# Kernel optimization log

Hardware: AMD Instinct MI355X
Metric: run time of the kernel (lower is better)

## Reference

```python
import jax, jax.numpy as jnp
import numpy as np

STRIDE = 1  # conv stride from __init__


def setup_inputs() -> dict:
    key = jax.random.key(0)
    k1, k2, k3 = jax.random.split(key, 3)
    prot1 = jax.random.normal(k1, (4, 1024, 8, 64), dtype=jnp.float32)
    prot2 = jax.random.normal(k2, (4, 1024, 8, 64), dtype=jnp.float32)
    # W: (no_filters, no_channels, no_dims, window_size)
    W = jax.random.normal(k3, (32, 8, 64, 7), dtype=jnp.float32)
    return {"prot1": prot1, "prot2": prot2, "W": W}


def _project(x, W, stride):
    """Fused equivalent of unfold + broadcast-mul + sum over (C, window).

    x: (N, H, C, D), W: (F, C, D, w) -> (N, F, H', D) with H' = (H - w)//stride + 1.
    This is a grouped 1D conv: D groups, each mixing C input channels into F outputs.
    """
    N, H, C, D = x.shape
    Fn, _, _, w = W.shape
    xg = jnp.transpose(x, (0, 3, 2, 1)).reshape(N, D * C, H)        # (N, D*C, H)
    Wg = jnp.transpose(W, (2, 0, 1, 3)).reshape(D * Fn, C, w)       # (D*F, C, w)
    out = jax.lax.conv_general_dilated(
        xg, Wg, window_strides=(stride,), padding='VALID',
        dimension_numbers=('NCH', 'OIH', 'NCH'), feature_group_count=D)
    Hp = out.shape[-1]
    return jnp.transpose(out.reshape(N, D, Fn, Hp), (0, 2, 3, 1))   # (N, F, H', D)


def reference(prot1, prot2, W):
    q1 = _project(prot1, W, STRIDE)   # (N, F, H1', D)
    q2 = _project(prot2, W, STRIDE)   # (N, F, H2', D)
    H1p, H2p = q1.shape[2], q2.shape[2]
    scale = jnp.sqrt(jnp.asarray(H1p * H2p, dtype=q1.dtype))
    att = jnp.einsum('nfhd,nfgd->nfhg', q1, q2) / scale             # (N, F, H1', H2')
    a = jax.nn.softmax(att, axis=3)
    p1 = jnp.einsum('nfhg,nfgd->nfhd', a, q2)                       # (N, F, H1', D)
    # NB: source does transpose(att, 2, 2) (a no-op) and multiplies the SAME
    # softmax matrix by the UPDATED p1folds; we reproduce that faithfully.
    p2 = jnp.einsum('nfhg,nfgd->nfhd', a, p1)                       # (N, F, H1', D)
    out1 = jnp.tanh(jnp.transpose(p1, (0, 2, 1, 3)))                # (N, H1', F, D)
    out2 = jnp.tanh(jnp.transpose(p2, (0, 2, 1, 3)))
    # Dropout is identity in eval mode (and dropout_p=0.0 here).
    return (out1, out2)
```

## Files before the change

kernel.cpp:

```cpp
#include <hip/hip_runtime.h>
#include <math.h>

typedef __bf16 bf16_t;
typedef bf16_t bf16x4 __attribute__((ext_vector_type(4)));
typedef bf16_t bf16x8 __attribute__((ext_vector_type(8)));
typedef float  f32x16 __attribute__((ext_vector_type(16)));

#define HH 1024
#define CC 8
#define DD 64
#define FF 32
#define WW 7
#define HP 1018
#define HPAD 1024
#define NF 128
#define QOUT (NF*HP*DD)
#define QWS ((size_t)NF*HPAD*DD)

#if __has_builtin(__builtin_amdgcn_exp2f)
#define EXP2(x) __builtin_amdgcn_exp2f(x)
#else
#define EXP2(x) __expf((x) * 0.6931471805599453f)
#endif

__device__ __forceinline__ int vaddr(int row, int col) {
    return row*64 + ((((col>>3) ^ (row&7) ^ ((row>>2)&7)))<<3) + (col&7);
}

__global__ __launch_bounds__(256) void wprep_kernel(
    const float* __restrict__ Wt, float* __restrict__ Wp)
{
    const int idx = blockIdx.x * 256 + threadIdx.x;
    if (idx < FF*CC*DD*WW) {
        const int j = idx % WW;
        int t = idx / WW;
        const int d = t % DD; t /= DD;
        const int c = t % CC;
        const int f = t / CC;
        Wp[((f*CC + c)*WW + j)*DD + d] = Wt[idx];
    }
}

__global__ __launch_bounds__(256) void conv_kernel(
    const float* __restrict__ x1, const float* __restrict__ x2,
    const float* __restrict__ Wp, bf16_t* __restrict__ q1, bf16_t* __restrict__ q2)
{
    __shared__ float xs[38*512];
    const float* x = blockIdx.z ? x2 : x1;
    bf16_t* q = blockIdx.z ? q2 : q1;
    const int n = blockIdx.y;
    const int hb = blockIdx.x * 32;
    const int tid = threadIdx.x;

    const float4* xg = (const float4*)(x + (size_t)n*HH*512);
    for (int i = tid; i < 38*128; i += 256) {
        const int row = hb + (i >> 7);
        float4 v = {0.f, 0.f, 0.f, 0.f};
        if (row < HH) v = xg[(size_t)row*128 + (i & 127)];
        const int r = i >> 7;
        const int c = (i & 127) >> 4;
        const int d0 = ((i & 127) & 15) * 4;
        xs[r*512 + (d0+0)*8 + c] = v.x;
        xs[r*512 + (d0+1)*8 + c] = v.y;
        xs[r*512 + (d0+2)*8 + c] = v.z;
        xs[r*512 + (d0+3)*8 + c] = v.w;
    }
    __syncthreads();

    const int d = tid & 63;
    const int fq = tid >> 6;
    for (int fi = 0; fi < 8; ++fi) {
        const int f = fq*8 + fi;
        float w[CC][WW];
#pragma unroll
        for (int c = 0; c < CC; ++c)
#pragma unroll
            for (int j = 0; j < WW; ++j)
                w[c][j] = Wp[((f*CC + c)*WW + j)*DD + d];
#pragma unroll
        for (int hc = 0; hc < 2; ++hc) {
            float acc[16];
#pragma unroll
            for (int i = 0; i < 16; ++i) acc[i] = 0.f;
#pragma unroll
            for (int rr = 0; rr < 22; ++rr) {
                const float4 a = *(const float4*)&xs[(hc*16 + rr)*512 + d*8 + 0];
                const float4 b = *(const float4*)&xs[(hc*16 + rr)*512 + d*8 + 4];
                const float xv[8] = {a.x, a.y, a.z, a.w, b.x, b.y, b.z, b.w};
#pragma unroll
                for (int j = 0; j < WW; ++j) {
                    const int i = rr - j;
                    if (i >= 0 && i < 16) {
#pragma unroll
                        for (int c = 0; c < CC; ++c)
                            acc[i] = fmaf(xv[c], w[c][j], acc[i]);
                    }
                }
            }
#pragma unroll
            for (int i = 0; i < 16; ++i) {
                const int h = hb + hc*16 + i;
                const float v = (h < HP) ? acc[i] : 0.f;
                q[((size_t)(n*FF + f)*HPAD + h)*DD + d] = (bf16_t)v;
            }
        }
    }
}

__device__ __forceinline__ float fast_tanh(float x) {
    const float t = __expf(2.f * x);
    return (t - 1.f) / (t + 1.f);
}

template<int MODE>
__global__ __launch_bounds__(256, 2) void flash(
    const bf16_t* __restrict__ q1, const bf16_t* __restrict__ q2,
    const bf16_t* __restrict__ vsrc, bf16_t* __restrict__ p1out,
    float* __restrict__ out)
{
    __shared__ __align__(16) bf16_t Vt[64*64];

    const int head = blockIdx.y;
    const int n = head >> 5, f = head & 31;
    const int tid = threadIdx.x;
    const int w = tid >> 6;
    const int lane = tid & 63;
    const int lid = lane & 31;
    const int half = lane >> 5;
    const int hb = blockIdx.x * 256 + w * 64;

    const size_t qoff = (size_t)head * HPAD * DD;
    const float SC = 1.442695041f / 1018.f;
    const int vswz = (lid & 7) ^ (lid >> 2);

    const int gq = tid >> 4;
    const int dq = tid & 15;
    const int cgb = 4*((gq>>1)&1) + 8*(gq&1) + 16*(gq>>2);

    const bf16_t* vptr = (MODE == 1) ? vsrc : q2;

    bf16x8 bq1[2][4];
#pragma unroll
    for (int nt = 0; nt < 2; ++nt)
#pragma unroll
        for (int kt = 0; kt < 4; ++kt)
            bq1[nt][kt] = *(const bf16x8*)&q1[qoff + (size_t)(hb + 32*nt + lid)*DD + 16*kt + 8*half];

    bf16x8 aq[2][4];
#pragma unroll
    for (int mt = 0; mt < 2; ++mt)
#pragma unroll
        for (int kt = 0; kt < 4; ++kt)
            aq[mt][kt] = *(const bf16x8*)&q2[qoff + (size_t)(32*mt + lid)*DD + 16*kt + 8*half];

    bf16x4 rV[4];
#pragma unroll
    for (int i = 0; i < 4; ++i)
        rV[i] = *(const bf16x4*)&vptr[qoff + (size_t)(4*gq + i)*DD + 4*dq];

    f32x16 O[2][2] = {};
    float lacc[2] = {0.f, 0.f};

    for (int g0 = 0; g0 < HPAD; g0 += 64) {
        __syncthreads();
#pragma unroll
        for (int j = 0; j < 4; ++j) {
            bf16x4 c = { rV[0][j], rV[1][j], rV[2][j], rV[3][j] };
            *(bf16x4*)&Vt[vaddr(4*dq + j, cgb)] = c;
        }
        __syncthreads();

        if (g0 + 64 < HPAD) {
#pragma unroll
            for (int i = 0; i < 4; ++i)
                rV[i] = *(const bf16x4*)&vptr[qoff + (size_t)(g0 + 64 + 4*gq + i)*DD + 4*dq];
        }

        const bool tail = (g0 + 64 > HP);

#pragma unroll
        for (int mt = 0; mt < 2; ++mt) {
            f32x16 C[2] = {};
#pragma unroll
            for (int kt = 0; kt < 4; ++kt) {
                C[0] = __builtin_amdgcn_mfma_f32_32x32x16_bf16(aq[mt][kt], bq1[0][kt], C[0], 0,0,0);
                C[1] = __builtin_amdgcn_mfma_f32_32x32x16_bf16(aq[mt][kt], bq1[1][kt], C[1], 0,0,0);
            }
            if (g0 + 64 < HPAD) {
#pragma unroll
                for (int kt = 0; kt < 4; ++kt)
                    aq[mt][kt] = *(const bf16x8*)&q2[qoff + (size_t)(g0 + 64 + 32*mt + lid)*DD + 16*kt + 8*half];
            }
            bf16x8 af[2][2];
#pragma unroll
            for (int nt = 0; nt < 2; ++nt) {
                float ls = 0.f;
#pragma unroll
                for (int s = 0; s < 16; ++s) {
                    float e = EXP2(C[nt][s] * SC);
                    if (tail) {
                        const int gg = g0 + 32*mt + (s&3) + 8*(s>>2) + 4*half;
                        if (gg >= HP) e = 0.f;
                    }
                    ls += e;
                    af[nt][s>>3][s&7] = (bf16_t)e;
                }
                lacc[nt] += ls;
            }
#pragma unroll
            for (int u = 0; u < 2; ++u) {
#pragma unroll
                for (int dt = 0; dt < 2; ++dt) {
                    const int chunk = (4*mt + 2*u + half) ^ vswz;
                    bf16x8 b = *(const bf16x8*)&Vt[(32*dt + lid)*64 + chunk*8];
                    O[0][dt] = __builtin_amdgcn_mfma_f32_32x32x16_bf16(af[0][u], b, O[0][dt], 0,0,0);
                    O[1][dt] = __builtin_amdgcn_mfma_f32_32x32x16_bf16(af[1][u], b, O[1][dt], 0,0,0);
                }
            }
        }
    }

    float linv[2];
#pragma unroll
    for (int nt = 0; nt < 2; ++nt) {
        const float l = lacc[nt] + __shfl_xor(lacc[nt], 32);
        linv[nt] = 1.f / l;
    }
#pragma unroll
    for (int ht = 0; ht < 2; ++ht) {
#pragma unroll
        for (int s = 0; s < 16; ++s) {
            const int R = (s&3) + 8*(s>>2) + 4*half;
            const float li = __shfl(linv[ht], R);
            const int hg = hb + 32*ht + R;
#pragma unroll
            for (int dt = 0; dt < 2; ++dt) {
                const int d = 32*dt + lid;
                const float val = O[ht][dt][s] * li;
                if (hg < HP)
                    out[(((size_t)n*HP + hg)*FF + f)*DD + d] = fast_tanh(val);
                if (MODE == 0)
                    p1out[qoff + (size_t)hg*DD + d] = (bf16_t)(hg < HP ? val : 0.f);
            }
        }
    }
}

extern "C" void kernel_launch(void* const* d_in, const int* in_sizes, int n_in,
                              void* d_out, int out_size, void* d_ws, size_t ws_size,
                              hipStream_t stream)
{
    const float* prot1 = (const float*)d_in[0];
    const float* prot2 = (const float*)d_in[1];
    const float* Wt    = (const float*)d_in[2];
    float* out = (float*)d_out;

    bf16_t* q1b = (bf16_t*)d_ws;
    bf16_t* q2b = q1b + QWS;
    bf16_t* p1b = q2b + QWS;
    float* Wp   = (float*)(p1b + QWS);

    wprep_kernel<<<dim3(448), 256, 0, stream>>>(Wt, Wp);
    conv_kernel<<<dim3(32, 4, 2), 256, 0, stream>>>(prot1, prot2, Wp, q1b, q2b);
    flash<0><<<dim3(4, NF), 256, 0, stream>>>(q1b, q2b, q2b, p1b, out);
    flash<1><<<dim3(4, NF), 256, 0, stream>>>(q1b, q2b, p1b, p1b, out + QOUT);
}
```

Baseline: 220.6 us.

## Double-buffer V tiles, compute row sums via MFMA, prescale q1 in conv

The flash kernel now processes 128 keys per iteration with double-buffered shared-memory V tiles, which removes one barrier per step and prefetches further ahead. Softmax row sums are accumulated with an MFMA against a ones vector instead of scalar adds and cross-lane shuffles. The exp2 scale factor is folded into q1 in the conv kernel. The conv grid is doubled so each block computes two filters at once with more register reuse. In exchange, shared memory use and register pressure go up, and the prescaled bf16 q1 carries slightly different rounding.

```diff
diff --git a/kernel.cpp b/kernel.cpp
--- a/kernel.cpp
+++ b/kernel.cpp
@@ -16,6 +16,7 @@
 #define NF 128
 #define QOUT (NF*HP*DD)
 #define QWS ((size_t)NF*HPAD*DD)
+#define SCEXP (1.442695041f/1018.f)
 
 #if __has_builtin(__builtin_amdgcn_exp2f)
 #define EXP2(x) __builtin_amdgcn_exp2f(x)
@@ -48,8 +49,10 @@
     __shared__ float xs[38*512];
     const float* x = blockIdx.z ? x2 : x1;
     bf16_t* q = blockIdx.z ? q2 : q1;
+    const float qscale = blockIdx.z ? 1.0f : SCEXP;
     const int n = blockIdx.y;
-    const int hb = blockIdx.x * 32;
+    const int hb = (blockIdx.x >> 1) * 32;
+    const int fh = (blockIdx.x & 1) * 4;
     const int tid = threadIdx.x;
 
     const float4* xg = (const float4*)(x + (size_t)n*HH*512);
@@ -69,19 +72,23 @@
 
     const int d = tid & 63;
     const int fq = tid >> 6;
-    for (int fi = 0; fi < 8; ++fi) {
-        const int f = fq*8 + fi;
-        float w[CC][WW];
-#pragma unroll
-        for (int c = 0; c < CC; ++c)
-#pragma unroll
-            for (int j = 0; j < WW; ++j)
-                w[c][j] = Wp[((f*CC + c)*WW + j)*DD + d];
+    for (int fp = 0; fp < 2; ++fp) {
+        const int f0 = fq*8 + fh + fp*2;
+        float w[2][CC][WW];
+#pragma unroll
+        for (int e = 0; e < 2; ++e)
+#pragma unroll
+            for (int c = 0; c < CC; ++c)
+#pragma unroll
+                for (int j = 0; j < WW; ++j)
+                    w[e][c][j] = Wp[(((f0+e)*CC + c)*WW + j)*DD + d];
 #pragma unroll
         for (int hc = 0; hc < 2; ++hc) {
-            float acc[16];
-#pragma unroll
-            for (int i = 0; i < 16; ++i) acc[i] = 0.f;
+            float acc[2][16];
+#pragma unroll
+            for (int e = 0; e < 2; ++e)
+#pragma unroll
+                for (int i = 0; i < 16; ++i) acc[e][i] = 0.f;
 #pragma unroll
             for (int rr = 0; rr < 22; ++rr) {
                 const float4 a = *(const float4*)&xs[(hc*16 + rr)*512 + d*8 + 0];
@@ -92,18 +99,22 @@
                     const int i = rr - j;
                     if (i >= 0 && i < 16) {
 #pragma unroll
-                        for (int c = 0; c < CC; ++c)
-                            acc[i] = fmaf(xv[c], w[c][j], acc[i]);
+                        for (int c = 0; c < CC; ++c) {
+                            acc[0][i] = fmaf(xv[c], w[0][c][j], acc[0][i]);
+                            acc[1][i] = fmaf(xv[c], w[1][c][j], acc[1][i]);
+                        }
                     }
                 }
             }
 #pragma unroll
-            for (int i = 0; i < 16; ++i) {
-                const int h = hb + hc*16 + i;
-                const float v = (h < HP) ? acc[i] : 0.f;
-                q[((size_t)(n*FF + f)*HPAD + h)*DD + d] = (bf16_t)v;
-            }
-        }
+            for (int e = 0; e < 2; ++e)
+#pragma unroll
+                for (int i = 0; i < 16; ++i) {
+                    const int h = hb + hc*16 + i;
+                    const float v = (h < HP) ? acc[e][i] * qscale : 0.f;
+                    q[((size_t)(n*FF + f0 + e)*HPAD + h)*DD + d] = (bf16_t)v;
+                }
+    }
     }
 }
 
@@ -118,7 +129,7 @@
     const bf16_t* __restrict__ vsrc, bf16_t* __restrict__ p1out,
     float* __restrict__ out)
 {
-    __shared__ __align__(16) bf16_t Vt[64*64];
+    __shared__ __align__(16) bf16_t Vt[2][2][64*64];
 
     const int head = blockIdx.y;
     const int n = head >> 5, f = head & 31;
@@ -130,7 +141,6 @@
     const int hb = blockIdx.x * 256 + w * 64;
 
     const size_t qoff = (size_t)head * HPAD * DD;
-    const float SC = 1.442695041f / 1018.f;
     const int vswz = (lid & 7) ^ (lid >> 2);
 
     const int gq = tid >> 4;
@@ -146,97 +156,122 @@
         for (int kt = 0; kt < 4; ++kt)
             bq1[nt][kt] = *(const bf16x8*)&q1[qoff + (size_t)(hb + 32*nt + lid)*DD + 16*kt + 8*half];
 
-    bf16x8 aq[2][4];
-#pragma unroll
-    for (int mt = 0; mt < 2; ++mt)
-#pragma unroll
-        for (int kt = 0; kt < 4; ++kt)
-            aq[mt][kt] = *(const bf16x8*)&q2[qoff + (size_t)(32*mt + lid)*DD + 16*kt + 8*half];
-
-    bf16x4 rV[4];
-#pragma unroll
-    for (int i = 0; i < 4; ++i)
-        rV[i] = *(const bf16x4*)&vptr[qoff + (size_t)(4*gq + i)*DD + 4*dq];
+    bf16x8 onesb;
+#pragma unroll
+    for (int j = 0; j < 8; ++j) onesb[j] = (bf16_t)1.0f;
 
     f32x16 O[2][2] = {};
-    float lacc[2] = {0.f, 0.f};
-
-    for (int g0 = 0; g0 < HPAD; g0 += 64) {
+    f32x16 lO[2]   = {};
+
+    bf16x4 rV[2][4];
+#pragma unroll
+    for (int t = 0; t < 2; ++t)
+#pragma unroll
+        for (int i = 0; i < 4; ++i)
+            rV[t][i] = *(const bf16x4*)&vptr[qoff + (size_t)(t*64 + 4*gq + i)*DD + 4*dq];
+#pragma unroll
+    for (int t = 0; t < 2; ++t)
+#pragma unroll
+        for (int j = 0; j < 4; ++j) {
+            bf16x4 c = {rV[t][0][j], rV[t][1][j], rV[t][2][j], rV[t][3][j]};
+            *(bf16x4*)&Vt[0][t][vaddr(4*dq + j, cgb)] = c;
+        }
+#pragma unroll
+    for (int t = 0; t < 2; ++t)
+#pragma unroll
+        for (int i = 0; i < 4; ++i)
+            rV[t][i] = *(const bf16x4*)&vptr[qoff + (size_t)(128 + t*64 + 4*gq + i)*DD + 4*dq];
+
+    bf16x8 aq[2][2][4];
+#pragma unroll
+    for (int t = 0; t < 2; ++t)
+#pragma unroll
+        for (int mt = 0; mt < 2; ++mt)
+#pragma unroll
+            for (int kt = 0; kt < 4; ++kt)
+                aq[t][mt][kt] = *(const bf16x8*)&q2[qoff + (size_t)(t*64 + 32*mt + lid)*DD + 16*kt + 8*half];
+
+    for (int it = 0; it < 8; ++it) {
         __syncthreads();
-#pragma unroll
-        for (int j = 0; j < 4; ++j) {
-            bf16x4 c = { rV[0][j], rV[1][j], rV[2][j], rV[3][j] };
-            *(bf16x4*)&Vt[vaddr(4*dq + j, cgb)] = c;
-        }
-        __syncthreads();
-
-        if (g0 + 64 < HPAD) {
-#pragma unroll
-            for (int i = 0; i < 4; ++i)
-                rV[i] = *(const bf16x4*)&vptr[qoff + (size_t)(g0 + 64 + 4*gq + i)*DD + 4*dq];
-        }
-
-        const bool tail = (g0 + 64 > HP);
-
-#pragma unroll
-        for (int mt = 0; mt < 2; ++mt) {
-            f32x16 C[2] = {};
-#pragma unroll
-            for (int kt = 0; kt < 4; ++kt) {
-                C[0] = __builtin_amdgcn_mfma_f32_32x32x16_bf16(aq[mt][kt], bq1[0][kt], C[0], 0,0,0);
-                C[1] = __builtin_amdgcn_mfma_f32_32x32x16_bf16(aq[mt][kt], bq1[1][kt], C[1], 0,0,0);
+        const int cur = it & 1;
+        if (it < 7) {
+#pragma unroll
+            for (int t = 0; t < 2; ++t)
+#pragma unroll
+                for (int j = 0; j < 4; ++j) {
+                    bf16x4 c = {rV[t][0][j], rV[t][1][j], rV[t][2][j], rV[t][3][j]};
+                    *(bf16x4*)&Vt[cur^1][t][vaddr(4*dq + j, cgb)] = c;
+                }
+        }
+        if (it < 6) {
+            const int base = (it + 2) * 128;
+#pragma unroll
+            for (int t = 0; t < 2; ++t)
+#pragma unroll
+                for (int i = 0; i < 4; ++i)
+                    rV[t][i] = *(const bf16x4*)&vptr[qoff + (size_t)(base + t*64 + 4*gq + i)*DD + 4*dq];
+        }
+#pragma unroll
+        for (int t = 0; t < 2; ++t) {
+            const int g0 = it*128 + t*64;
+            const bool tail = (g0 + 64 > HP);
+#pragma unroll
+            for (int mt = 0; mt < 2; ++mt) {
+                f32x16 C[2] = {};
+#pragma unroll
+                for (int kt = 0; kt < 4; ++kt) {
+                    C[0] = __builtin_amdgcn_mfma_f32_32x32x16_bf16(aq[t][mt][kt], bq1[0][kt], C[0], 0,0,0);
+                    C[1] = __builtin_amdgcn_mfma_f32_32x32x16_bf16(aq[t][mt][kt], bq1[1][kt], C[1], 0,0,0);
+                }
+                if (it < 7) {
+                    const int nb = (it + 1) * 128;
+#pragma unroll
+                    for (int kt = 0; kt < 4; ++kt)
+                        aq[t][mt][kt] = *(const bf16x8*)&q2[qoff + (size_t)(nb + t*64 + 32*mt + lid)*DD + 16*kt + 8*half];
+                }
+                bf16x8 af[2][2];
+#pragma unroll
+                for (int nt = 0; nt < 2; ++nt) {
+#pragma unroll
+                    for (int s = 0; s < 16; ++s) {
+                        float e = EXP2((float)C[nt][s]);
+                        if (tail) {
+                            const int gg = g0 + 32*mt + (s&3) + 8*(s>>2) + 4*half;
+                            if (gg >= HP) e = 0.f;
+                        }
+                        af[nt][s>>3][s&7] = (bf16_t)e;
+                    }
+                }
+#pragma unroll
+                for (int u = 0; u < 2; ++u) {
+                    lO[0] = __builtin_amdgcn_mfma_f32_32x32x16_bf16(af[0][u], onesb, lO[0], 0,0,0);
+                    lO[1] = __builtin_amdgcn_mfma_f32_32x32x16_bf16(af[1][u], onesb, lO[1], 0,0,0);
+                }
+#pragma unroll
+                for (int u = 0; u < 2; ++u) {
+#pragma unroll
+                    for (int dt = 0; dt < 2; ++dt) {
+                        const int chunk = (4*mt + 2*u + half) ^ vswz;
+                        bf16x8 b = *(const bf16x8*)&Vt[cur][t][(32*dt + lid)*64 + chunk*8];
+                        O[0][dt] = __builtin_amdgcn_mfma_f32_32x32x16_bf16(af[0][u], b, O[0][dt], 0,0,0);
+                        O[1][dt] = __builtin_amdgcn_mfma_f32_32x32x16_bf16(af[1][u], b, O[1][dt], 0,0,0);
+                    }
+                }
             }
-            if (g0 + 64 < HPAD) {
-#pragma unroll
-                for (int kt = 0; kt < 4; ++kt)
-                    aq[mt][kt] = *(const bf16x8*)&q2[qoff + (size_t)(g0 + 64 + 32*mt + lid)*DD + 16*kt + 8*half];
-            }
-            bf16x8 af[2][2];
-#pragma unroll
-            for (int nt = 0; nt < 2; ++nt) {
-                float ls = 0.f;
-#pragma unroll
-                for (int s = 0; s < 16; ++s) {
-                    float e = EXP2(C[nt][s] * SC);
-                    if (tail) {
-                        const int gg = g0 + 32*mt + (s&3) + 8*(s>>2) + 4*half;
-                        if (gg >= HP) e = 0.f;
-                    }
-                    ls += e;
-                    af[nt][s>>3][s&7] = (bf16_t)e;
-                }
-                lacc[nt] += ls;
-            }
-#pragma unroll
-            for (int u = 0; u < 2; ++u) {
-#pragma unroll
-                for (int dt = 0; dt < 2; ++dt) {
-                    const int chunk = (4*mt + 2*u + half) ^ vswz;
-                    bf16x8 b = *(const bf16x8*)&Vt[(32*dt + lid)*64 + chunk*8];
-                    O[0][dt] = __builtin_amdgcn_mfma_f32_32x32x16_bf16(af[0][u], b, O[0][dt], 0,0,0);
-                    O[1][dt] = __builtin_amdgcn_mfma_f32_32x32x16_bf16(af[1][u], b, O[1][dt], 0,0,0);
-                }
-            }
-        }
-    }
-
-    float linv[2];
-#pragma unroll
-    for (int nt = 0; nt < 2; ++nt) {
-        const float l = lacc[nt] + __shfl_xor(lacc[nt], 32);
-        linv[nt] = 1.f / l;
-    }
+        }
+    }
+
 #pragma unroll
     for (int ht = 0; ht < 2; ++ht) {
 #pragma unroll
         for (int s = 0; s < 16; ++s) {
             const int R = (s&3) + 8*(s>>2) + 4*half;
-            const float li = __shfl(linv[ht], R);
             const int hg = hb + 32*ht + R;
+            const float linv = 1.f / lO[ht][s];
 #pragma unroll
             for (int dt = 0; dt < 2; ++dt) {
                 const int d = 32*dt + lid;
-                const float val = O[ht][dt][s] * li;
+                const float val = O[ht][dt][s] * linv;
                 if (hg < HP)
                     out[(((size_t)n*HP + hg)*FF + f)*DD + d] = fast_tanh(val);
                 if (MODE == 0)
@@ -261,7 +296,7 @@
     float* Wp   = (float*)(p1b + QWS);
 
     wprep_kernel<<<dim3(448), 256, 0, stream>>>(Wt, Wp);
-    conv_kernel<<<dim3(32, 4, 2), 256, 0, stream>>>(prot1, prot2, Wp, q1b, q2b);
+    conv_kernel<<<dim3(64, 4, 2), 256, 0, stream>>>(prot1, prot2, Wp, q1b, q2b);
     flash<0><<<dim3(4, NF), 256, 0, stream>>>(q1b, q2b, q2b, p1b, out);
     flash<1><<<dim3(4, NF), 256, 0, stream>>>(q1b, q2b, p1b, p1b, out + QOUT);
 }
```

Measured after the change: 316.1 us. +43.3%, slower.

## Pre-transpose input to bf16, fold softmax scale into conv, MFMA row sums

Applied to the files above, without the earlier changes.

Adds a prep kernel that transposes the inputs to a (row, d, c) bf16 layout so the conv kernel loads contiguous 16-byte vectors. The conv tile shrinks to 16 rows, doubling the grid, and the log2e/scale factor is folded into q1 at conv time, so the flash kernel's exp2 takes raw logits. Softmax row sums are now computed by an MFMA against a ones vector instead of scalar adds plus shuffles. The costs are an extra kernel launch and a workspace round trip, bf16 rounding of the raw inputs, and more MFMA work per tile.

```diff
diff --git a/kernel.cpp b/kernel.cpp
--- a/kernel.cpp
+++ b/kernel.cpp
@@ -16,6 +16,7 @@
 #define NF 128
 #define QOUT (NF*HP*DD)
 #define QWS ((size_t)NF*HPAD*DD)
+#define SCEXP (1.442695041f/1018.f)
 
 #if __has_builtin(__builtin_amdgcn_exp2f)
 #define EXP2(x) __builtin_amdgcn_exp2f(x)
@@ -41,29 +42,57 @@
     }
 }
 
+__global__ __launch_bounds__(256) void xprep_kernel(
+    const float* __restrict__ x1, const float* __restrict__ x2,
+    bf16_t* __restrict__ xt)
+{
+    __shared__ float ls[8][CC][DD+1];
+    const float* x = blockIdx.z ? x2 : x1;
+    bf16_t* o = xt + (size_t)blockIdx.z * (4*HH*512);
+    const int n = blockIdx.y;
+    const int r0 = blockIdx.x * 8;
+    const int tid = threadIdx.x;
+
+#pragma unroll
+    for (int it = 0; it < 4; ++it) {
+        const int i = it*256 + tid;
+        const int r = i >> 7;
+        const int idx = i & 127;
+        const int c = idx >> 4;
+        const int d0 = (idx & 15) * 4;
+        float4 v = *(const float4*)&x[((size_t)(n*HH + r0 + r)*CC + c)*DD + d0];
+        ls[r][c][d0+0] = v.x; ls[r][c][d0+1] = v.y;
+        ls[r][c][d0+2] = v.z; ls[r][c][d0+3] = v.w;
+    }
+    __syncthreads();
+    const int d = tid & 63;
+    for (int r = (tid >> 6); r < 8; r += 4) {
+        bf16_t tmp[8];
+#pragma unroll
+        for (int c = 0; c < CC; ++c) tmp[c] = (bf16_t)ls[r][c][d];
+        *(bf16x8*)&o[((size_t)(n*HH + r0 + r)*DD + d)*CC] = *(bf16x8*)tmp;
+    }
+}
+
 __global__ __launch_bounds__(256) void conv_kernel(
-    const float* __restrict__ x1, const float* __restrict__ x2,
-    const float* __restrict__ Wp, bf16_t* __restrict__ q1, bf16_t* __restrict__ q2)
-{
-    __shared__ float xs[38*512];
-    const float* x = blockIdx.z ? x2 : x1;
-    bf16_t* q = blockIdx.z ? q2 : q1;
+    const bf16_t* __restrict__ xt, const float* __restrict__ Wp,
+    bf16_t* __restrict__ q1, bf16_t* __restrict__ q2)
+{
+    __shared__ __align__(16) bf16_t xs[22*64*8];
+    const int z = blockIdx.z;
+    const bf16_t* xb = xt + (size_t)z * (4*HH*512);
+    bf16_t* q = z ? q2 : q1;
+    const float qscale = z ? 1.0f : SCEXP;
     const int n = blockIdx.y;
-    const int hb = blockIdx.x * 32;
+    const int hb = blockIdx.x * 16;
     const int tid = threadIdx.x;
 
-    const float4* xg = (const float4*)(x + (size_t)n*HH*512);
-    for (int i = tid; i < 38*128; i += 256) {
-        const int row = hb + (i >> 7);
-        float4 v = {0.f, 0.f, 0.f, 0.f};
-        if (row < HH) v = xg[(size_t)row*128 + (i & 127)];
-        const int r = i >> 7;
-        const int c = (i & 127) >> 4;
-        const int d0 = ((i & 127) & 15) * 4;
-        xs[r*512 + (d0+0)*8 + c] = v.x;
-        xs[r*512 + (d0+1)*8 + c] = v.y;
-        xs[r*512 + (d0+2)*8 + c] = v.z;
-        xs[r*512 + (d0+3)*8 + c] = v.w;
+    for (int i = tid; i < 22*64; i += 256) {
+        const int row = hb + (i >> 6);
+        const int dd = i & 63;
+        bf16x8 v = {};
+        if (row < HH) v = *(const bf16x8*)&xb[((size_t)(n*HH + row)*DD + dd)*CC];
+        *(bf16x8*)&xs[(size_t)i*8] = v;
     }
     __syncthreads();
 
@@ -77,32 +106,30 @@
 #pragma unroll
             for (int j = 0; j < WW; ++j)
                 w[c][j] = Wp[((f*CC + c)*WW + j)*DD + d];
-#pragma unroll
-        for (int hc = 0; hc < 2; ++hc) {
-            float acc[16];
-#pragma unroll
-            for (int i = 0; i < 16; ++i) acc[i] = 0.f;
-#pragma unroll
-            for (int rr = 0; rr < 22; ++rr) {
-                const float4 a = *(const float4*)&xs[(hc*16 + rr)*512 + d*8 + 0];
-                const float4 b = *(const float4*)&xs[(hc*16 + rr)*512 + d*8 + 4];
-                const float xv[8] = {a.x, a.y, a.z, a.w, b.x, b.y, b.z, b.w};
-#pragma unroll
-                for (int j = 0; j < WW; ++j) {
-                    const int i = rr - j;
-                    if (i >= 0 && i < 16) {
-#pragma unroll
-                        for (int c = 0; c < CC; ++c)
-                            acc[i] = fmaf(xv[c], w[c][j], acc[i]);
-                    }
+        float acc[16];
+#pragma unroll
+        for (int i = 0; i < 16; ++i) acc[i] = 0.f;
+#pragma unroll
+        for (int rr = 0; rr < 22; ++rr) {
+            bf16x8 xv8 = *(const bf16x8*)&xs[(rr*64 + d)*8];
+            float xv[8];
+#pragma unroll
+            for (int c = 0; c < CC; ++c) xv[c] = (float)xv8[c];
+#pragma unroll
+            for (int j = 0; j < WW; ++j) {
+                const int i = rr - j;
+                if (i >= 0 && i < 16) {
+#pragma unroll
+                    for (int c = 0; c < CC; ++c)
+                        acc[i] = fmaf(xv[c], w[c][j], acc[i]);
                 }
             }
-#pragma unroll
-            for (int i = 0; i < 16; ++i) {
-                const int h = hb + hc*16 + i;
-                const float v = (h < HP) ? acc[i] : 0.f;
-                q[((size_t)(n*FF + f)*HPAD + h)*DD + d] = (bf16_t)v;
-            }
+        }
+#pragma unroll
+        for (int i = 0; i < 16; ++i) {
+            const int h = hb + i;
+            const float v = (h < HP) ? acc[i] * qscale : 0.f;
+            q[((size_t)(n*FF + f)*HPAD + h)*DD + d] = (bf16_t)v;
         }
     }
 }
@@ -130,7 +157,6 @@
     const int hb = blockIdx.x * 256 + w * 64;
 
     const size_t qoff = (size_t)head * HPAD * DD;
-    const float SC = 1.442695041f / 1018.f;
     const int vswz = (lid & 7) ^ (lid >> 2);
 
     const int gq = tid >> 4;
@@ -146,6 +172,10 @@
         for (int kt = 0; kt < 4; ++kt)
             bq1[nt][kt] = *(const bf16x8*)&q1[qoff + (size_t)(hb + 32*nt + lid)*DD + 16*kt + 8*half];
 
+    bf16x8 onesb;
+#pragma unroll
+    for (int j = 0; j < 8; ++j) onesb[j] = (bf16_t)1.0f;
+
     bf16x8 aq[2][4];
 #pragma unroll
     for (int mt = 0; mt < 2; ++mt)
@@ -159,7 +189,7 @@
         rV[i] = *(const bf16x4*)&vptr[qoff + (size_t)(4*gq + i)*DD + 4*dq];
 
     f32x16 O[2][2] = {};
-    float lacc[2] = {0.f, 0.f};
+    f32x16 lO[2] = {};
 
     for (int g0 = 0; g0 < HPAD; g0 += 64) {
         __syncthreads();
@@ -194,18 +224,20 @@
             bf16x8 af[2][2];
 #pragma unroll
             for (int nt = 0; nt < 2; ++nt) {
-                float ls = 0.f;
 #pragma unroll
                 for (int s = 0; s < 16; ++s) {
-                    float e = EXP2(C[nt][s] * SC);
+                    float e = EXP2((float)C[nt][s]);
                     if (tail) {
                         const int gg = g0 + 32*mt + (s&3) + 8*(s>>2) + 4*half;
                         if (gg >= HP) e = 0.f;
                     }
-                    ls += e;
                     af[nt][s>>3][s&7] = (bf16_t)e;
                 }
-                lacc[nt] += ls;
+            }
+#pragma unroll
+            for (int u = 0; u < 2; ++u) {
+                lO[0] = __builtin_amdgcn_mfma_f32_32x32x16_bf16(af[0][u], onesb, lO[0], 0,0,0);
+                lO[1] = __builtin_amdgcn_mfma_f32_32x32x16_bf16(af[1][u], onesb, lO[1], 0,0,0);
             }
 #pragma unroll
             for (int u = 0; u < 2; ++u) {
@@ -220,23 +252,17 @@
         }
     }
 
-    float linv[2];
-#pragma unroll
-    for (int nt = 0; nt < 2; ++nt) {
-        const float l = lacc[nt] + __shfl_xor(lacc[nt], 32);
-        linv[nt] = 1.f / l;
-    }
 #pragma unroll
     for (int ht = 0; ht < 2; ++ht) {
 #pragma unroll
         for (int s = 0; s < 16; ++s) {
             const int R = (s&3) + 8*(s>>2) + 4*half;
-            const float li = __shfl(linv[ht], R);
             const int hg = hb + 32*ht + R;
+            const float linv = 1.f / lO[ht][s];
 #pragma unroll
             for (int dt = 0; dt < 2; ++dt) {
                 const int d = 32*dt + lid;
-                const float val = O[ht][dt][s] * li;
+                const float val = O[ht][dt][s] * linv;
                 if (hg < HP)
                     out[(((size_t)n*HP + hg)*FF + f)*DD + d] = fast_tanh(val);
                 if (MODE == 0)
@@ -258,10 +284,12 @@
     bf16_t* q1b = (bf16_t*)d_ws;
     bf16_t* q2b = q1b + QWS;
     bf16_t* p1b = q2b + QWS;
-    float* Wp   = (float*)(p1b + QWS);
+    float*  Wp  = (float*)(p1b + QWS);
+    bf16_t* xtb = (bf16_t*)(Wp + FF*CC*DD*WW);
 
     wprep_kernel<<<dim3(448), 256, 0, stream>>>(Wt, Wp);
-    conv_kernel<<<dim3(32, 4, 2), 256, 0, stream>>>(prot1, prot2, Wp, q1b, q2b);
+    xprep_kernel<<<dim3(HH/8, 4, 2), 256, 0, stream>>>(prot1, prot2, xtb);
+    conv_kernel<<<dim3(64, 4, 2), 256, 0, stream>>>(xtb, Wp, q1b, q2b);
     flash<0><<<dim3(4, NF), 256, 0, stream>>>(q1b, q2b, q2b, p1b, out);
     flash<1><<<dim3(4, NF), 256, 0, stream>>>(q1b, q2b, p1b, p1b, out + QOUT);
 }
```

Result: slower. 248.5 us (+12.7%).
